# Optimization experiments

Measured on AMD Instinct MI355X. Metric: run time of the kernel, lower is better.

The kernel has to match this reference:

```python
import jax, jax.numpy as jnp
import numpy as np

BATCH = 4096
MAX_ATOMS = 1024


def setup_inputs() -> dict:
    key = jax.random.key(0)
    k1, k2, k3 = jax.random.split(key, 3)
    inp = jax.random.normal(k1, (BATCH, 3 * MAX_ATOMS), dtype=jnp.float32)
    tgt = jax.random.normal(k2, (BATCH, 3 * MAX_ATOMS), dtype=jnp.float32)
    num_atoms = jax.random.randint(k3, (BATCH,), 8, MAX_ATOMS + 1, dtype=jnp.int32)
    return {"input": inp, "target": tgt, "num_atoms": num_atoms}


def _kabsch_rmsd(inp, tgt, num_atoms):
    B = inp.shape[0]
    N = inp.shape[1] // 3
    x = inp.reshape(B, N, 3)
    y = tgt.reshape(B, N, 3)
    # mask out padded atoms (atom index >= num_atoms)
    mask = (jnp.arange(N)[None, :] < num_atoms[:, None])[..., None]  # [B,N,1]
    n = num_atoms.astype(x.dtype)[:, None, None]                      # [B,1,1]
    xm = jnp.where(mask, x, 0.0)
    ym = jnp.where(mask, y, 0.0)
    # center on masked centroid; keep padded rows exactly zero
    xc = jnp.where(mask, xm - xm.sum(axis=1, keepdims=True) / n, 0.0)
    yc = jnp.where(mask, ym - ym.sum(axis=1, keepdims=True) / n, 0.0)
    # 3x3 covariance per sample
    R = jnp.einsum("bni,bnj->bij", xc, yc)
    U, S, Vt = jnp.linalg.svd(R)
    # proper-rotation (reflection) correction
    d = jnp.sign(jnp.linalg.det(U) * jnp.linalg.det(Vt))
    s = S[:, 0] + S[:, 1] + d * S[:, 2]
    e = (jnp.sum(xc * xc, axis=(1, 2)) + jnp.sum(yc * yc, axis=(1, 2)) - 2.0 * s)
    msd = e / num_atoms.astype(e.dtype)
    return jnp.sqrt(jnp.maximum(msd, 1e-12))


def reference(input, target, num_atoms):
    return _kabsch_rmsd(input, target, num_atoms)
```

## Files before the change

kernel.cpp:

```cpp
#include <hip/hip_runtime.h>
#include <math.h>

constexpr int NATOMS = 1024;

__device__ __forceinline__ float wred(float v) {
#pragma unroll
    for (int o = 32; o > 0; o >>= 1) v += __shfl_xor(v, o, 64);
    return v;
}

__global__ __launch_bounds__(256) void rmsd_kernel(
    const float* __restrict__ inp, const float* __restrict__ tgt,
    const int* __restrict__ natoms, float* __restrict__ out)
{
    const int b = blockIdx.x;
    const int t = threadIdx.x;
    const int n = natoms[b];

    const float4* __restrict__ x4 = (const float4*)(inp + (size_t)b * (3 * NATOMS)) + t * 3;
    const float4* __restrict__ y4 = (const float4*)(tgt + (size_t)b * (3 * NATOMS)) + t * 3;

    float4 xa = x4[0], xb = x4[1], xc = x4[2];
    float4 ya = y4[0], yb = y4[1], yc = y4[2];

    float acc[17];
#pragma unroll
    for (int i = 0; i < 17; ++i) acc[i] = 0.f;

    const float X[4][3] = {{xa.x,xa.y,xa.z},{xa.w,xb.x,xb.y},{xb.z,xb.w,xc.x},{xc.y,xc.z,xc.w}};
    const float Y[4][3] = {{ya.x,ya.y,ya.z},{ya.w,yb.x,yb.y},{yb.z,yb.w,yc.x},{yc.y,yc.z,yc.w}};
    const int base = t * 4;
#pragma unroll
    for (int j = 0; j < 4; ++j) {
        const float m = (base + j < n) ? 1.f : 0.f;
        const float x0 = X[j][0]*m, x1 = X[j][1]*m, x2 = X[j][2]*m;
        const float y0 = Y[j][0]*m, y1 = Y[j][1]*m, y2 = Y[j][2]*m;
        acc[0] += x0; acc[1] += x1; acc[2] += x2;
        acc[3] += y0; acc[4] += y1; acc[5] += y2;
        acc[6]  += x0*y0; acc[7]  += x0*y1; acc[8]  += x0*y2;
        acc[9]  += x1*y0; acc[10] += x1*y1; acc[11] += x1*y2;
        acc[12] += x2*y0; acc[13] += x2*y1; acc[14] += x2*y2;
        acc[15] += x0*x0 + x1*x1 + x2*x2;
        acc[16] += y0*y0 + y1*y1 + y2*y2;
    }

#pragma unroll
    for (int i = 0; i < 17; ++i) acc[i] = wred(acc[i]);

    __shared__ float red[4][17];
    const int wave = t >> 6, lane = t & 63;
    if (lane == 0) {
#pragma unroll
        for (int i = 0; i < 17; ++i) red[wave][i] = acc[i];
    }
    __syncthreads();

    if (t == 0) {
        double s[17];
#pragma unroll
        for (int i = 0; i < 17; ++i)
            s[i] = (double)red[0][i] + (double)red[1][i] + (double)red[2][i] + (double)red[3][i];
        const double nd = (double)n;

        double R[3][3];
        for (int i = 0; i < 3; ++i)
            for (int j = 0; j < 3; ++j)
                R[i][j] = s[6 + i*3 + j] - s[i] * s[3 + j] / nd;
        const double ex = s[15] - (s[0]*s[0] + s[1]*s[1] + s[2]*s[2]) / nd;
        const double ey = s[16] - (s[3]*s[3] + s[4]*s[4] + s[5]*s[5]) / nd;

        const double detR =
              R[0][0]*(R[1][1]*R[2][2] - R[1][2]*R[2][1])
            - R[0][1]*(R[1][0]*R[2][2] - R[1][2]*R[2][0])
            + R[0][2]*(R[1][0]*R[2][1] - R[1][1]*R[2][0]);

        double K00=0, K01=0, K02=0, K11=0, K12=0, K22=0;
        for (int k = 0; k < 3; ++k) {
            K00 += R[k][0]*R[k][0]; K01 += R[k][0]*R[k][1]; K02 += R[k][0]*R[k][2];
            K11 += R[k][1]*R[k][1]; K12 += R[k][1]*R[k][2]; K22 += R[k][2]*R[k][2];
        }

        const double qm = (K00 + K11 + K22) / 3.0;
        const double p1 = K01*K01 + K02*K02 + K12*K12;
        const double p2 = (K00-qm)*(K00-qm) + (K11-qm)*(K11-qm) + (K22-qm)*(K22-qm) + 2.0*p1;
        double e1, e2, e3;
        if (p2 <= 1e-30) {
            e1 = e2 = e3 = qm;
        } else {
            const double p = sqrt(p2 / 6.0);
            const double inv = 1.0 / p;
            const double B00 = (K00-qm)*inv, B11 = (K11-qm)*inv, B22 = (K22-qm)*inv;
            const double B01 = K01*inv, B02 = K02*inv, B12 = K12*inv;
            const double detB =
                  B00*(B11*B22 - B12*B12)
                - B01*(B01*B22 - B12*B02)
                + B02*(B01*B12 - B11*B02);
            double r = detB * 0.5;
            r = fmin(1.0, fmax(-1.0, r));
            const double phi = acos(r) / 3.0;
            e1 = qm + 2.0*p*cos(phi);
            e3 = qm + 2.0*p*cos(phi + 2.0943951023931953);
            e2 = 3.0*qm - e1 - e3;
        }
        const double S1 = sqrt(fmax(e1, 0.0));
        const double S2 = sqrt(fmax(e2, 0.0));
        const double S3 = sqrt(fmax(e3, 0.0));
        const double dsg = (detR < 0.0) ? -1.0 : 1.0;
        const double sv = S1 + S2 + dsg * S3;

        const double e = ex + ey - 2.0 * sv;
        out[b] = (float)sqrt(fmax(e / nd, 1e-12));
    }
}

extern "C" void kernel_launch(void* const* d_in, const int* in_sizes, int n_in,
                              void* d_out, int out_size, void* d_ws, size_t ws_size,
                              hipStream_t stream) {
    const float* inp = (const float*)d_in[0];
    const float* tgt = (const float*)d_in[1];
    const int*   na  = (const int*)d_in[2];
    float* out = (float*)d_out;
    const int batch = in_sizes[2];
    rmsd_kernel<<<batch, 256, 0, stream>>>(inp, tgt, na, out);
}
```

Before: 119.2 us.

## Split into per-wave reduction kernel and batched per-thread 3x3 SVD solve kernel

Each wave now handles one sample: it loops over four 256-atom chunks, skips chunks beyond num_atoms so padded data is never loaded, and writes 16 partial sums to the workspace. A second kernel solves the 3x3 eigenproblem in double precision with one thread per sample, replacing the single serial thread per block. The two squared-norm sums are merged into one. The cost is an extra kernel launch and a workspace round trip.

```diff
diff --git a/kernel.cpp b/kernel.cpp
--- a/kernel.cpp
+++ b/kernel.cpp
@@ -9,108 +9,128 @@
     return v;
 }
 
-__global__ __launch_bounds__(256) void rmsd_kernel(
+__global__ __launch_bounds__(256) void rmsd_reduce(
     const float* __restrict__ inp, const float* __restrict__ tgt,
-    const int* __restrict__ natoms, float* __restrict__ out)
+    const int* __restrict__ natoms, float* __restrict__ ws, int batch)
 {
-    const int b = blockIdx.x;
-    const int t = threadIdx.x;
+    const int wave = threadIdx.x >> 6;
+    const int lane = threadIdx.x & 63;
+    const int b = blockIdx.x * 4 + wave;
+    if (b >= batch) return;
     const int n = natoms[b];
 
-    const float4* __restrict__ x4 = (const float4*)(inp + (size_t)b * (3 * NATOMS)) + t * 3;
-    const float4* __restrict__ y4 = (const float4*)(tgt + (size_t)b * (3 * NATOMS)) + t * 3;
+    const float4* __restrict__ x0 = (const float4*)(inp + (size_t)b * (3 * NATOMS));
+    const float4* __restrict__ y0 = (const float4*)(tgt + (size_t)b * (3 * NATOMS));
 
-    float4 xa = x4[0], xb = x4[1], xc = x4[2];
-    float4 ya = y4[0], yb = y4[1], yc = y4[2];
+    float acc[16];
+#pragma unroll
+    for (int i = 0; i < 16; ++i) acc[i] = 0.f;
 
-    float acc[17];
 #pragma unroll
-    for (int i = 0; i < 17; ++i) acc[i] = 0.f;
-
-    const float X[4][3] = {{xa.x,xa.y,xa.z},{xa.w,xb.x,xb.y},{xb.z,xb.w,xc.x},{xc.y,xc.z,xc.w}};
-    const float Y[4][3] = {{ya.x,ya.y,ya.z},{ya.w,yb.x,yb.y},{yb.z,yb.w,yc.x},{yc.y,yc.z,yc.w}};
-    const int base = t * 4;
+    for (int c = 0; c < 4; ++c) {
+        const int cbase = c * 256;
+        if (cbase < n) {
+            const float4* x4 = x0 + c * 192 + lane * 3;
+            const float4* y4 = y0 + c * 192 + lane * 3;
+            float4 xa = x4[0], xb = x4[1], xc = x4[2];
+            float4 ya = y4[0], yb = y4[1], yc = y4[2];
+            const float X[4][3] = {{xa.x,xa.y,xa.z},{xa.w,xb.x,xb.y},{xb.z,xb.w,xc.x},{xc.y,xc.z,xc.w}};
+            const float Y[4][3] = {{ya.x,ya.y,ya.z},{ya.w,yb.x,yb.y},{yb.z,yb.w,yc.x},{yc.y,yc.z,yc.w}};
+            const int abase = cbase + lane * 4;
 #pragma unroll
-    for (int j = 0; j < 4; ++j) {
-        const float m = (base + j < n) ? 1.f : 0.f;
-        const float x0 = X[j][0]*m, x1 = X[j][1]*m, x2 = X[j][2]*m;
-        const float y0 = Y[j][0]*m, y1 = Y[j][1]*m, y2 = Y[j][2]*m;
-        acc[0] += x0; acc[1] += x1; acc[2] += x2;
-        acc[3] += y0; acc[4] += y1; acc[5] += y2;
-        acc[6]  += x0*y0; acc[7]  += x0*y1; acc[8]  += x0*y2;
-        acc[9]  += x1*y0; acc[10] += x1*y1; acc[11] += x1*y2;
-        acc[12] += x2*y0; acc[13] += x2*y1; acc[14] += x2*y2;
-        acc[15] += x0*x0 + x1*x1 + x2*x2;
-        acc[16] += y0*y0 + y1*y1 + y2*y2;
+            for (int j = 0; j < 4; ++j) {
+                const float m = (abase + j < n) ? 1.f : 0.f;
+                const float p0 = X[j][0]*m, p1 = X[j][1]*m, p2 = X[j][2]*m;
+                const float q0 = Y[j][0]*m, q1 = Y[j][1]*m, q2 = Y[j][2]*m;
+                acc[0] += p0; acc[1] += p1; acc[2] += p2;
+                acc[3] += q0; acc[4] += q1; acc[5] += q2;
+                acc[6]  += p0*q0; acc[7]  += p0*q1; acc[8]  += p0*q2;
+                acc[9]  += p1*q0; acc[10] += p1*q1; acc[11] += p1*q2;
+                acc[12] += p2*q0; acc[13] += p2*q1; acc[14] += p2*q2;
+                acc[15] += p0*p0 + p1*p1 + p2*p2 + q0*q0 + q1*q1 + q2*q2;
+            }
+        }
     }
 
 #pragma unroll
-    for (int i = 0; i < 17; ++i) acc[i] = wred(acc[i]);
+    for (int i = 0; i < 16; ++i) acc[i] = wred(acc[i]);
 
-    __shared__ float red[4][17];
-    const int wave = t >> 6, lane = t & 63;
     if (lane == 0) {
-#pragma unroll
-        for (int i = 0; i < 17; ++i) red[wave][i] = acc[i];
+        float4* o = (float4*)(ws + (size_t)b * 16);
+        o[0] = make_float4(acc[0],  acc[1],  acc[2],  acc[3]);
+        o[1] = make_float4(acc[4],  acc[5],  acc[6],  acc[7]);
+        o[2] = make_float4(acc[8],  acc[9],  acc[10], acc[11]);
+        o[3] = make_float4(acc[12], acc[13], acc[14], acc[15]);
     }
-    __syncthreads();
+}
 
-    if (t == 0) {
-        double s[17];
-#pragma unroll
-        for (int i = 0; i < 17; ++i)
-            s[i] = (double)red[0][i] + (double)red[1][i] + (double)red[2][i] + (double)red[3][i];
-        const double nd = (double)n;
+__global__ __launch_bounds__(256) void rmsd_solve(
+    const float* __restrict__ ws, const int* __restrict__ natoms,
+    float* __restrict__ out, int batch)
+{
+    const int b = blockIdx.x * 256 + threadIdx.x;
+    if (b >= batch) return;
+    const int n = natoms[b];
 
-        double R[3][3];
-        for (int i = 0; i < 3; ++i)
-            for (int j = 0; j < 3; ++j)
-                R[i][j] = s[6 + i*3 + j] - s[i] * s[3 + j] / nd;
-        const double ex = s[15] - (s[0]*s[0] + s[1]*s[1] + s[2]*s[2]) / nd;
-        const double ey = s[16] - (s[3]*s[3] + s[4]*s[4] + s[5]*s[5]) / nd;
+    const float4* s4 = (const float4*)(ws + (size_t)b * 16);
+    const float4 v0 = s4[0], v1 = s4[1], v2 = s4[2], v3 = s4[3];
+    const double sx0 = v0.x, sx1 = v0.y, sx2 = v0.z;
+    const double sy0 = v0.w, sy1 = v1.x, sy2 = v1.y;
+    const double c00 = v1.z, c01 = v1.w, c02 = v2.x;
+    const double c10 = v2.y, c11 = v2.z, c12 = v2.w;
+    const double c20 = v3.x, c21 = v3.y, c22 = v3.z;
+    const double sq  = v3.w;
 
-        const double detR =
-              R[0][0]*(R[1][1]*R[2][2] - R[1][2]*R[2][1])
-            - R[0][1]*(R[1][0]*R[2][2] - R[1][2]*R[2][0])
-            + R[0][2]*(R[1][0]*R[2][1] - R[1][1]*R[2][0]);
+    const double nd = (double)n;
+    const double inv = 1.0 / nd;
 
-        double K00=0, K01=0, K02=0, K11=0, K12=0, K22=0;
-        for (int k = 0; k < 3; ++k) {
-            K00 += R[k][0]*R[k][0]; K01 += R[k][0]*R[k][1]; K02 += R[k][0]*R[k][2];
-            K11 += R[k][1]*R[k][1]; K12 += R[k][1]*R[k][2]; K22 += R[k][2]*R[k][2];
-        }
+    double R[3][3];
+    R[0][0] = c00 - sx0*sy0*inv; R[0][1] = c01 - sx0*sy1*inv; R[0][2] = c02 - sx0*sy2*inv;
+    R[1][0] = c10 - sx1*sy0*inv; R[1][1] = c11 - sx1*sy1*inv; R[1][2] = c12 - sx1*sy2*inv;
+    R[2][0] = c20 - sx2*sy0*inv; R[2][1] = c21 - sx2*sy1*inv; R[2][2] = c22 - sx2*sy2*inv;
+    const double exy = sq - (sx0*sx0 + sx1*sx1 + sx2*sx2 + sy0*sy0 + sy1*sy1 + sy2*sy2) * inv;
 
-        const double qm = (K00 + K11 + K22) / 3.0;
-        const double p1 = K01*K01 + K02*K02 + K12*K12;
-        const double p2 = (K00-qm)*(K00-qm) + (K11-qm)*(K11-qm) + (K22-qm)*(K22-qm) + 2.0*p1;
-        double e1, e2, e3;
-        if (p2 <= 1e-30) {
-            e1 = e2 = e3 = qm;
-        } else {
-            const double p = sqrt(p2 / 6.0);
-            const double inv = 1.0 / p;
-            const double B00 = (K00-qm)*inv, B11 = (K11-qm)*inv, B22 = (K22-qm)*inv;
-            const double B01 = K01*inv, B02 = K02*inv, B12 = K12*inv;
-            const double detB =
-                  B00*(B11*B22 - B12*B12)
-                - B01*(B01*B22 - B12*B02)
-                + B02*(B01*B12 - B11*B02);
-            double r = detB * 0.5;
-            r = fmin(1.0, fmax(-1.0, r));
-            const double phi = acos(r) / 3.0;
-            e1 = qm + 2.0*p*cos(phi);
-            e3 = qm + 2.0*p*cos(phi + 2.0943951023931953);
-            e2 = 3.0*qm - e1 - e3;
-        }
-        const double S1 = sqrt(fmax(e1, 0.0));
-        const double S2 = sqrt(fmax(e2, 0.0));
-        const double S3 = sqrt(fmax(e3, 0.0));
-        const double dsg = (detR < 0.0) ? -1.0 : 1.0;
-        const double sv = S1 + S2 + dsg * S3;
+    const double detR =
+          R[0][0]*(R[1][1]*R[2][2] - R[1][2]*R[2][1])
+        - R[0][1]*(R[1][0]*R[2][2] - R[1][2]*R[2][0])
+        + R[0][2]*(R[1][0]*R[2][1] - R[1][1]*R[2][0]);
 
-        const double e = ex + ey - 2.0 * sv;
-        out[b] = (float)sqrt(fmax(e / nd, 1e-12));
+    double K00=0, K01=0, K02=0, K11=0, K12=0, K22=0;
+    for (int k = 0; k < 3; ++k) {
+        K00 += R[k][0]*R[k][0]; K01 += R[k][0]*R[k][1]; K02 += R[k][0]*R[k][2];
+        K11 += R[k][1]*R[k][1]; K12 += R[k][1]*R[k][2]; K22 += R[k][2]*R[k][2];
     }
+
+    const double qm = (K00 + K11 + K22) / 3.0;
+    const double p1 = K01*K01 + K02*K02 + K12*K12;
+    const double p2 = (K00-qm)*(K00-qm) + (K11-qm)*(K11-qm) + (K22-qm)*(K22-qm) + 2.0*p1;
+    double e1, e2, e3;
+    if (p2 <= 1e-30) {
+        e1 = e2 = e3 = qm;
+    } else {
+        const double p = sqrt(p2 / 6.0);
+        const double pinv = 1.0 / p;
+        const double B00 = (K00-qm)*pinv, B11 = (K11-qm)*pinv, B22 = (K22-qm)*pinv;
+        const double B01 = K01*pinv, B02 = K02*pinv, B12 = K12*pinv;
+        const double detB =
+              B00*(B11*B22 - B12*B12)
+            - B01*(B01*B22 - B12*B02)
+            + B02*(B01*B12 - B11*B02);
+        double r = detB * 0.5;
+        r = fmin(1.0, fmax(-1.0, r));
+        const double phi = acos(r) / 3.0;
+        e1 = qm + 2.0*p*cos(phi);
+        e3 = qm + 2.0*p*cos(phi + 2.0943951023931953);
+        e2 = 3.0*qm - e1 - e3;
+    }
+    const double S1 = sqrt(fmax(e1, 0.0));
+    const double S2 = sqrt(fmax(e2, 0.0));
+    const double S3 = sqrt(fmax(e3, 0.0));
+    const double dsg = (detR < 0.0) ? -1.0 : 1.0;
+    const double sv = S1 + S2 + dsg * S3;
+
+    const double e = exy - 2.0 * sv;
+    out[b] = (float)sqrt(fmax(e * inv, 1e-12));
 }
 
 extern "C" void kernel_launch(void* const* d_in, const int* in_sizes, int n_in,
@@ -120,6 +140,9 @@
     const float* tgt = (const float*)d_in[1];
     const int*   na  = (const int*)d_in[2];
     float* out = (float*)d_out;
+    float* ws  = (float*)d_ws;
     const int batch = in_sizes[2];
-    rmsd_kernel<<<batch, 256, 0, stream>>>(inp, tgt, na, out);
+
+    rmsd_reduce<<<(batch + 3) / 4, 256, 0, stream>>>(inp, tgt, na, ws, batch);
+    rmsd_solve<<<(batch + 255) / 256, 256, 0, stream>>>(ws, na, out, batch);
 }
```

After: 115.9 us. 1.03x faster.
